# Kernel tuning notes

Measured on AMD Instinct MI355X. Metric: run time of the kernel, lower is better.

## Reference

```python
import jax, jax.numpy as jnp
import numpy as np
import math

FACTOR = 5

def setup_inputs() -> dict:
    key = jax.random.key(0)
    k1, k2, k3, k4 = jax.random.split(key, 4)
    B, L, H, D = 2, 4096, 8, 64
    sample_k = min(FACTOR * int(np.ceil(np.log(L))), L)  # 45
    return {
        "queries": jax.random.normal(k1, (B, L, H, D), dtype=jnp.float32),
        "keys": jax.random.normal(k2, (B, L, H, D), dtype=jnp.float32),
        "values": jax.random.normal(k3, (B, L, H, D), dtype=jnp.float32),
        "attn_mask": jnp.zeros((1,), dtype=bool),  # unused (mask_flag=False)
        "index_sample": jax.random.randint(k4, (L, sample_k), 0, L, dtype=jnp.int64),
    }

def reference(queries, keys, values, attn_mask, index_sample):
    B, L_Q, H, D = queries.shape
    L_K = keys.shape[1]
    # [B,L,H,D] -> [B,H,L,D]
    q = jnp.transpose(queries, (0, 2, 1, 3))
    k = jnp.transpose(keys, (0, 2, 1, 3))
    v = jnp.transpose(values, (0, 2, 1, 3))

    n_top = min(FACTOR * int(np.ceil(np.log(L_Q))), L_Q)  # u

    # --- _prob_QK ---
    # K_sample[b,h,l,s,e] = k[b,h,index_sample[l,s],e]
    K_sample = k[:, :, index_sample, :]                      # [B,H,L_Q,S,E]
    Q_K_sample = jnp.einsum('bhle,bhlse->bhls', q, K_sample)  # [B,H,L_Q,S]
    # sparsity measure: max - mean(over full L_K as in torch code)
    M = Q_K_sample.max(axis=-1) - Q_K_sample.sum(axis=-1) / L_K  # [B,H,L_Q]
    M_top = jax.lax.top_k(M, n_top)[1]                        # [B,H,u] indices

    Q_reduce = jnp.take_along_axis(q, M_top[..., None], axis=2)  # [B,H,u,E]
    scores_top = jnp.einsum('bhue,bhke->bhuk', Q_reduce, k)      # [B,H,u,L_K]

    scale = 1.0 / math.sqrt(D)
    attn = jax.nn.softmax(scale * scores_top, axis=-1)           # [B,H,u,L_K]
    context_in_q = jnp.einsum('bhuk,bhkd->bhud', attn, v)        # [B,H,u,D]

    # scatter selected contexts into zero-initialized tensor
    b_idx = jnp.arange(B)[:, None, None]
    h_idx = jnp.arange(H)[None, :, None]
    context = jnp.zeros((B, H, L_Q, D), dtype=queries.dtype)
    context = context.at[b_idx, h_idx, M_top].set(context_in_q)

    return jnp.transpose(context, (0, 2, 1, 3))  # [B,L_Q,H,D]
```

## Files before the change

### kernel.cpp

```cpp
#include <hip/hip_runtime.h>
#include <math.h>

#define B_ 2
#define L_ 4096
#define H_ 8
#define D_ 64
#define S_ 45
#define NTOP_ 45
#define SCALE 0.125f
#define TKEYS 64
#define NSPLIT 64

template<int CTRL>
__device__ __forceinline__ float dpp_permf(float x) {
    return __int_as_float(__builtin_amdgcn_update_dpp(
        0, __float_as_int(x), CTRL, 0xF, 0xF, true));
}

__global__ __launch_bounds__(256) void compute_M_kernel(
    const float* __restrict__ q, const float* __restrict__ k,
    const int* __restrict__ samp, float* __restrict__ M) {
    __shared__ int sIdx[8 * 48];
    int tid = threadIdx.x;
    int g   = blockIdx.x;
    int xcd = g & 7;
    int chunk = g >> 3;
    int b  = xcd >> 2;
    int h0 = (xcd & 3) * 2;
    int l0 = chunk * 8;

    for (int i = tid; i < 8 * S_; i += 256) {
        int qq = i / S_, ss = i - qq * S_;
        sIdx[qq * 48 + ss] = samp[(long)(l0 + qq) * S_ + ss];
    }
    if (tid < 24) sIdx[(tid / 3) * 48 + S_ + (tid % 3)] = 0;
    __syncthreads();

    int lane = tid & 63, wave = tid >> 6;
    int c  = lane & 31;
    int q8 = wave * 2 + (lane >> 5);
    int l  = l0 + q8;

    float4 q4 = ((const float4*)(q + (((long)(b * L_ + l)) * H_ + h0) * D_))[c];
    const float4* kb4 = (const float4*)(k + ((long)b * L_ * H_ + h0) * (long)D_);
    const int* myIdx = sIdx + q8 * 48;

    float4 f0 = kb4[(long)myIdx[0] * 128 + c];
    float4 f1 = kb4[(long)myIdx[1] * 128 + c];
    float4 f2 = kb4[(long)myIdx[2] * 128 + c];

    float vmax = -INFINITY, vsum = 0.f;
    #pragma unroll 3
    for (int s = 0; s < S_; ++s) {
        float4 nf = kb4[(long)myIdx[s + 3] * 128 + c];
        float p = q4.x * f0.x + q4.y * f0.y + q4.z * f0.z + q4.w * f0.w;
        p += dpp_permf<0xB1>(p);
        p += dpp_permf<0x4E>(p);
        p += __shfl_xor(p, 4, 64);
        p += __shfl_xor(p, 8, 64);
        vmax = fmaxf(vmax, p);
        vsum += p;
        f0 = f1; f1 = f2; f2 = nf;
    }
    if ((lane & 15) == 0) {
        int h = h0 + ((lane >> 4) & 1);
        M[(long)(b * 8 + h) * L_ + l] = vmax - vsum * (1.0f / (float)L_);
    }
}

__global__ __launch_bounds__(256) void chunk_topk_kernel(
    const float* __restrict__ M, unsigned long long* __restrict__ cand) {
    __shared__ unsigned long long sKey[256];
    int g = blockIdx.x;
    int bh = g >> 4, chunk = g & 15;
    int tid = threadIdx.x;
    int l = chunk * 256 + tid;
    unsigned int bts = __float_as_uint(M[(long)bh * L_ + l]);
    unsigned int mapped = bts ^ ((unsigned int)((int)bts >> 31) | 0x80000000u);
    unsigned long long key =
        ((unsigned long long)mapped << 32) | (unsigned long long)(0xFFFFFFFFu - (unsigned int)l);
    sKey[tid] = key;
    __syncthreads();
    int rank = 0;
    #pragma unroll 16
    for (int j = 0; j < 256; ++j)
        rank += (sKey[j] > key) ? 1 : 0;
    if (rank < NTOP_)
        cand[((long)bh * 16 + chunk) * NTOP_ + rank] = key;
}

__global__ __launch_bounds__(256) void merge_topk_kernel(
    const unsigned long long* __restrict__ cand, int* __restrict__ topIdx) {
    __shared__ unsigned long long sKey[16 * NTOP_];
    int bh = blockIdx.x, tid = threadIdx.x;
    for (int i = tid; i < 16 * NTOP_; i += 256)
        sKey[i] = cand[(long)bh * 16 * NTOP_ + i];
    __syncthreads();
    unsigned long long k0 = sKey[tid];
    unsigned long long k1 = sKey[tid + 256];
    bool has2 = (tid + 512) < 16 * NTOP_;
    unsigned long long k2 = has2 ? sKey[tid + 512] : 0ull;
    int r0 = 0, r1 = 0, r2 = 0;
    #pragma unroll 8
    for (int j = 0; j < 16 * NTOP_; ++j) {
        unsigned long long kj = sKey[j];
        r0 += (kj > k0) ? 1 : 0;
        r1 += (kj > k1) ? 1 : 0;
        r2 += (kj > k2) ? 1 : 0;
    }
    int* outRow = topIdx + bh * NTOP_;
    if (r0 < NTOP_) outRow[r0] = (int)(0xFFFFFFFFu - (unsigned int)(k0 & 0xFFFFFFFFull));
    if (r1 < NTOP_) outRow[r1] = (int)(0xFFFFFFFFu - (unsigned int)(k1 & 0xFFFFFFFFull));
    if (has2 && r2 < NTOP_) outRow[r2] = (int)(0xFFFFFFFFu - (unsigned int)(k2 & 0xFFFFFFFFull));
}

#define STRIDE 68
__global__ __launch_bounds__(256, 2) void attn_strip_kernel(
    const float* __restrict__ q, const float* __restrict__ k,
    const float* __restrict__ v, const int* __restrict__ topIdx,
    float* __restrict__ pOut, float* __restrict__ plPart, int nsplit) {
    __shared__ float sQ[48 * STRIDE];
    __shared__ float sK[TKEYS * STRIDE];
    __shared__ float sV[TKEYS * STRIDE];
    __shared__ float sP[48 * STRIDE];

    int g = blockIdx.x;
    int xcd = g & 7;
    int s0 = g >> 3;
    int grp = s0 / nsplit;
    int bh = xcd + 8 * grp;
    int split = s0 - grp * nsplit;
    int b = bh >> 3, h = bh & 7;
    int tid = threadIdx.x;
    int key0 = split * TKEYS;

    #pragma unroll
    for (int j = 0; j < 3; ++j) {
        int i = tid + 256 * j;
        int u = i >> 4, d4 = i & 15;
        float4 val = make_float4(0.f, 0.f, 0.f, 0.f);
        if (u < NTOP_) {
            int lq = topIdx[bh * NTOP_ + u];
            val = *(const float4*)(q + (((long)(b * L_ + lq)) * H_ + h) * D_ + 4 * d4);
        }
        *(float4*)(sQ + u * STRIDE + 4 * d4) = val;
    }
    #pragma unroll
    for (int j = 0; j < 4; ++j) {
        int i = tid + 256 * j;
        int r = i >> 4, d4 = i & 15;
        long off = (((long)(b * L_ + key0 + r)) * H_ + h) * D_ + 4 * d4;
        *(float4*)(sK + r * STRIDE + 4 * d4) = *(const float4*)(k + off);
        *(float4*)(sV + r * STRIDE + 4 * d4) = *(const float4*)(v + off);
    }
    __syncthreads();

    int tx = tid & 15, ty = tid >> 4;
    float acc[3][4];
    #pragma unroll
    for (int i = 0; i < 3; ++i)
        #pragma unroll
        for (int j = 0; j < 4; ++j) acc[i][j] = 0.f;

    #pragma unroll 4
    for (int d4 = 0; d4 < 16; ++d4) {
        float4 qv[3];
        #pragma unroll
        for (int i = 0; i < 3; ++i)
            qv[i] = *(const float4*)(sQ + (3 * ty + i) * STRIDE + 4 * d4);
        #pragma unroll
        for (int j = 0; j < 4; ++j) {
            float4 kv = *(const float4*)(sK + (tx + 16 * j) * STRIDE + 4 * d4);
            #pragma unroll
            for (int i = 0; i < 3; ++i)
                acc[i][j] += qv[i].x * kv.x + qv[i].y * kv.y + qv[i].z * kv.z + qv[i].w * kv.w;
        }
    }
    #pragma unroll
    for (int i = 0; i < 3; ++i) {
        #pragma unroll
        for (int j = 0; j < 4; ++j)
            sP[(3 * ty + i) * STRIDE + tx + 16 * j] = __expf(acc[i][j] * SCALE);
    }
    __syncthreads();

    int dx = tid & 15, uy = tid >> 4;
    float o[3][4];
    float ls[3];
    #pragma unroll
    for (int i = 0; i < 3; ++i) {
        ls[i] = 0.f;
        #pragma unroll
        for (int c = 0; c < 4; ++c) o[i][c] = 0.f;
    }
    #pragma unroll 4
    for (int k4 = 0; k4 < 16; ++k4) {
        float pa[3][4];
        #pragma unroll
        for (int i = 0; i < 3; ++i)
            *(float4*)pa[i] = *(const float4*)(sP + (3 * uy + i) * STRIDE + 4 * k4);
        #pragma unroll
        for (int c = 0; c < 4; ++c) {
            float4 vr = *(const float4*)(sV + (4 * k4 + c) * STRIDE + 4 * dx);
            #pragma unroll
            for (int i = 0; i < 3; ++i) {
                o[i][0] += pa[i][c] * vr.x;
                o[i][1] += pa[i][c] * vr.y;
                o[i][2] += pa[i][c] * vr.z;
                o[i][3] += pa[i][c] * vr.w;
                ls[i]   += pa[i][c];
            }
        }
    }
    #pragma unroll
    for (int i = 0; i < 3; ++i) {
        int u = 3 * uy + i;
        if (u < NTOP_) {
            long base = ((long)(split * 16 + bh) * NTOP_ + u) * D_;
            *(float4*)(pOut + base + 4 * dx) = make_float4(o[i][0], o[i][1], o[i][2], o[i][3]);
            if (dx == 0) plPart[(long)(split * 16 + bh) * NTOP_ + u] = ls[i];
        }
    }
}

__global__ __launch_bounds__(256) void zero_reduce_scatter_kernel(
    const int* __restrict__ topIdx, const float* __restrict__ pOut,
    const float* __restrict__ plPart, float* __restrict__ out, int nsplit) {
    __shared__ int sTop[8 * NTOP_];
    __shared__ int sel[256];
    __shared__ int selCnt;
    int g = blockIdx.x;
    int b = g >> 7;
    int l0 = (g & 127) * 32;
    int tid = threadIdx.x;
    if (tid == 0) selCnt = 0;
    for (int i = tid; i < 8 * NTOP_; i += 256) sTop[i] = topIdx[b * 8 * NTOP_ + i];
    __syncthreads();

    float4* obase = (float4*)(out + ((long)(b * L_ + l0)) * H_ * D_);
    float4 z = make_float4(0.f, 0.f, 0.f, 0.f);
    #pragma unroll
    for (int j = 0; j < 16; ++j) obase[tid + 256 * j] = z;

    {
        int l = l0 + (tid >> 3), h = tid & 7;
        const int* rowp = sTop + h * NTOP_;
        int u = -1;
        #pragma unroll
        for (int t = 0; t < NTOP_; ++t)
            if (rowp[t] == l) u = t;
        if (u >= 0) { int p = atomicAdd(&selCnt, 1); sel[p] = (tid << 8) | u; }
    }
    __syncthreads();

    int lane = tid & 63, wave = tid >> 6;
    int n = selCnt;
    for (int w = wave; w < n; w += 4) {
        int e = sel[w];
        int t = e >> 8, u = e & 255;
        int l = l0 + (t >> 3), h = t & 7, bh = b * 8 + h;
        float lv = (lane < nsplit) ? plPart[((long)lane * 16 + bh) * NTOP_ + u] : 0.f;
        #pragma unroll
        for (int o = 32; o > 0; o >>= 1) lv += __shfl_xor(lv, o, 64);
        float accv = 0.f;
        const float* pb = pOut + ((long)bh * NTOP_ + u) * D_ + lane;
        #pragma unroll 8
        for (int s = 0; s < nsplit; ++s) accv += pb[(long)s * 16 * NTOP_ * D_];
        out[(((long)(b * L_ + l)) * H_ + h) * D_ + lane] = accv / lv;
    }
}

extern "C" void kernel_launch(void* const* d_in, const int* in_sizes, int n_in,
                              void* d_out, int out_size, void* d_ws, size_t ws_size,
                              hipStream_t stream) {
    const float* q = (const float*)d_in[0];
    const float* k = (const float*)d_in[1];
    const float* v = (const float*)d_in[2];
    const int* samp = (const int*)d_in[4];
    float* out = (float*)d_out;

    char* ws = (char*)d_ws;
    const size_t mBytes    = (size_t)B_ * H_ * L_ * sizeof(float);
    const size_t topBytes  = (size_t)B_ * H_ * NTOP_ * sizeof(int);
    const size_t plBytes   = (size_t)NSPLIT * 16 * NTOP_ * sizeof(float);
    const size_t poutBytes = (size_t)NSPLIT * 16 * NTOP_ * D_ * sizeof(float);
    float* M      = (float*)ws;
    int*   topIdx = (int*)(ws + mBytes);
    float* plPart = (float*)(ws + mBytes + topBytes);
    float* pOut   = (float*)(ws + mBytes + topBytes + plBytes);
    unsigned long long* cand =
        (unsigned long long*)(ws + mBytes + topBytes + plBytes + poutBytes);

    int nsplit = NSPLIT;
    while (nsplit > 1) {
        size_t need = mBytes + topBytes + plBytes +
                      (size_t)nsplit * 16 * NTOP_ * D_ * sizeof(float) +
                      (size_t)B_ * H_ * 16 * NTOP_ * sizeof(unsigned long long);
        if (need <= ws_size) break;
        nsplit >>= 1;
    }

    compute_M_kernel<<<4096, 256, 0, stream>>>(q, k, samp, M);

    chunk_topk_kernel<<<B_ * H_ * 16, 256, 0, stream>>>(M, cand);

    merge_topk_kernel<<<B_ * H_, 256, 0, stream>>>(cand, topIdx);

    attn_strip_kernel<<<nsplit * B_ * H_, 256, 0, stream>>>(
        q, k, v, topIdx, pOut, plPart, nsplit);

    zero_reduce_scatter_kernel<<<B_ * (L_ / 32), 256, 0, stream>>>(
        topIdx, pOut, plPart, out, nsplit);
}
```

Measured before the change: 172.6 us.

## Fold top-k merge into attention and reduce kernels, move output zeroing earlier

Removes the standalone merge_topk kernel. Each attention block and each reduce block now redoes the 720-candidate rank merge in shared memory, so the small serial merge launch drops out of the critical path. Zeroing of the output moves into the chunk top-k kernel. The reduce kernel is restructured per (b,h) so it only touches the selected rows and no longer scans for them. The cost is redundant merge work in 1024+64 blocks and extra shared memory in the attention kernel, which may lower occupancy.

```diff
diff --git a/kernel.cpp b/kernel.cpp
--- a/kernel.cpp
+++ b/kernel.cpp
@@ -10,6 +10,7 @@
 #define SCALE 0.125f
 #define TKEYS 64
 #define NSPLIT 64
+#define NCAND (16 * NTOP_)
 
 template<int CTRL>
 __device__ __forceinline__ float dpp_permf(float x) {
@@ -69,11 +70,18 @@
 }
 
 __global__ __launch_bounds__(256) void chunk_topk_kernel(
-    const float* __restrict__ M, unsigned long long* __restrict__ cand) {
+    const float* __restrict__ M, unsigned long long* __restrict__ cand,
+    float* __restrict__ out) {
     __shared__ unsigned long long sKey[256];
     int g = blockIdx.x;
     int bh = g >> 4, chunk = g & 15;
     int tid = threadIdx.x;
+
+    float4 z = make_float4(0.f, 0.f, 0.f, 0.f);
+    float4* obase = (float4*)out + (long)g * 4096 + tid;
+    #pragma unroll
+    for (int j = 0; j < 16; ++j) obase[j * 256] = z;
+
     int l = chunk * 256 + tid;
     unsigned int bts = __float_as_uint(M[(long)bh * L_ + l]);
     unsigned int mapped = bts ^ ((unsigned int)((int)bts >> 31) | 0x80000000u);
@@ -89,40 +97,41 @@
         cand[((long)bh * 16 + chunk) * NTOP_ + rank] = key;
 }
 
-__global__ __launch_bounds__(256) void merge_topk_kernel(
-    const unsigned long long* __restrict__ cand, int* __restrict__ topIdx) {
-    __shared__ unsigned long long sKey[16 * NTOP_];
-    int bh = blockIdx.x, tid = threadIdx.x;
-    for (int i = tid; i < 16 * NTOP_; i += 256)
-        sKey[i] = cand[(long)bh * 16 * NTOP_ + i];
+__device__ __forceinline__ void merge_topk_inline(
+    const unsigned long long* __restrict__ cand, int bh, int tid,
+    unsigned long long* sKey, int* sTop) {
+    for (int i = tid; i < NCAND; i += 256)
+        sKey[i] = cand[(long)bh * NCAND + i];
     __syncthreads();
     unsigned long long k0 = sKey[tid];
     unsigned long long k1 = sKey[tid + 256];
-    bool has2 = (tid + 512) < 16 * NTOP_;
+    bool has2 = (tid + 512) < NCAND;
     unsigned long long k2 = has2 ? sKey[tid + 512] : 0ull;
     int r0 = 0, r1 = 0, r2 = 0;
     #pragma unroll 8
-    for (int j = 0; j < 16 * NTOP_; ++j) {
+    for (int j = 0; j < NCAND; ++j) {
         unsigned long long kj = sKey[j];
         r0 += (kj > k0) ? 1 : 0;
         r1 += (kj > k1) ? 1 : 0;
         r2 += (kj > k2) ? 1 : 0;
     }
-    int* outRow = topIdx + bh * NTOP_;
-    if (r0 < NTOP_) outRow[r0] = (int)(0xFFFFFFFFu - (unsigned int)(k0 & 0xFFFFFFFFull));
-    if (r1 < NTOP_) outRow[r1] = (int)(0xFFFFFFFFu - (unsigned int)(k1 & 0xFFFFFFFFull));
-    if (has2 && r2 < NTOP_) outRow[r2] = (int)(0xFFFFFFFFu - (unsigned int)(k2 & 0xFFFFFFFFull));
+    if (r0 < NTOP_) sTop[r0] = (int)(0xFFFFFFFFu - (unsigned int)(k0 & 0xFFFFFFFFull));
+    if (r1 < NTOP_) sTop[r1] = (int)(0xFFFFFFFFu - (unsigned int)(k1 & 0xFFFFFFFFull));
+    if (has2 && r2 < NTOP_) sTop[r2] = (int)(0xFFFFFFFFu - (unsigned int)(k2 & 0xFFFFFFFFull));
+    __syncthreads();
 }
 
 #define STRIDE 68
 __global__ __launch_bounds__(256, 2) void attn_strip_kernel(
     const float* __restrict__ q, const float* __restrict__ k,
-    const float* __restrict__ v, const int* __restrict__ topIdx,
+    const float* __restrict__ v, const unsigned long long* __restrict__ cand,
     float* __restrict__ pOut, float* __restrict__ plPart, int nsplit) {
     __shared__ float sQ[48 * STRIDE];
     __shared__ float sK[TKEYS * STRIDE];
     __shared__ float sV[TKEYS * STRIDE];
     __shared__ float sP[48 * STRIDE];
+    __shared__ unsigned long long sKey[NCAND];
+    __shared__ int sTop[48];
 
     int g = blockIdx.x;
     int xcd = g & 7;
@@ -135,23 +144,26 @@
     int key0 = split * TKEYS;
 
     #pragma unroll
-    for (int j = 0; j < 3; ++j) {
-        int i = tid + 256 * j;
-        int u = i >> 4, d4 = i & 15;
-        float4 val = make_float4(0.f, 0.f, 0.f, 0.f);
-        if (u < NTOP_) {
-            int lq = topIdx[bh * NTOP_ + u];
-            val = *(const float4*)(q + (((long)(b * L_ + lq)) * H_ + h) * D_ + 4 * d4);
-        }
-        *(float4*)(sQ + u * STRIDE + 4 * d4) = val;
-    }
-    #pragma unroll
     for (int j = 0; j < 4; ++j) {
         int i = tid + 256 * j;
         int r = i >> 4, d4 = i & 15;
         long off = (((long)(b * L_ + key0 + r)) * H_ + h) * D_ + 4 * d4;
         *(float4*)(sK + r * STRIDE + 4 * d4) = *(const float4*)(k + off);
         *(float4*)(sV + r * STRIDE + 4 * d4) = *(const float4*)(v + off);
+    }
+
+    merge_topk_inline(cand, bh, tid, sKey, sTop);
+
+    #pragma unroll
+    for (int j = 0; j < 3; ++j) {
+        int i = tid + 256 * j;
+        int u = i >> 4, d4 = i & 15;
+        float4 val = make_float4(0.f, 0.f, 0.f, 0.f);
+        if (u < NTOP_) {
+            int lq = sTop[u];
+            val = *(const float4*)(q + (((long)(b * L_ + lq)) * H_ + h) * D_ + 4 * d4);
+        }
+        *(float4*)(sQ + u * STRIDE + 4 * d4) = val;
     }
     __syncthreads();
 
@@ -223,42 +235,23 @@
     }
 }
 
-__global__ __launch_bounds__(256) void zero_reduce_scatter_kernel(
-    const int* __restrict__ topIdx, const float* __restrict__ pOut,
+__global__ __launch_bounds__(256) void reduce_scatter_kernel(
+    const unsigned long long* __restrict__ cand, const float* __restrict__ pOut,
     const float* __restrict__ plPart, float* __restrict__ out, int nsplit) {
-    __shared__ int sTop[8 * NTOP_];
-    __shared__ int sel[256];
-    __shared__ int selCnt;
+    __shared__ unsigned long long sKey[NCAND];
+    __shared__ int sTop[48];
     int g = blockIdx.x;
-    int b = g >> 7;
-    int l0 = (g & 127) * 32;
+    int bh = g >> 2, rg = g & 3;
+    int b = bh >> 3, h = bh & 7;
     int tid = threadIdx.x;
-    if (tid == 0) selCnt = 0;
-    for (int i = tid; i < 8 * NTOP_; i += 256) sTop[i] = topIdx[b * 8 * NTOP_ + i];
-    __syncthreads();
-
-    float4* obase = (float4*)(out + ((long)(b * L_ + l0)) * H_ * D_);
-    float4 z = make_float4(0.f, 0.f, 0.f, 0.f);
-    #pragma unroll
-    for (int j = 0; j < 16; ++j) obase[tid + 256 * j] = z;
-
-    {
-        int l = l0 + (tid >> 3), h = tid & 7;
-        const int* rowp = sTop + h * NTOP_;
-        int u = -1;
-        #pragma unroll
-        for (int t = 0; t < NTOP_; ++t)
-            if (rowp[t] == l) u = t;
-        if (u >= 0) { int p = atomicAdd(&selCnt, 1); sel[p] = (tid << 8) | u; }
-    }
-    __syncthreads();
+
+    merge_topk_inline(cand, bh, tid, sKey, sTop);
 
     int lane = tid & 63, wave = tid >> 6;
-    int n = selCnt;
-    for (int w = wave; w < n; w += 4) {
-        int e = sel[w];
-        int t = e >> 8, u = e & 255;
-        int l = l0 + (t >> 3), h = t & 7, bh = b * 8 + h;
+    #pragma unroll
+    for (int it = 0; it < 3; ++it) {
+        int u = rg * 12 + it * 4 + wave;
+        if (u >= NTOP_ || u >= rg * 12 + 12) continue;
         float lv = (lane < nsplit) ? plPart[((long)lane * 16 + bh) * NTOP_ + u] : 0.f;
         #pragma unroll
         for (int o = 32; o > 0; o >>= 1) lv += __shfl_xor(lv, o, 64);
@@ -266,6 +259,7 @@
         const float* pb = pOut + ((long)bh * NTOP_ + u) * D_ + lane;
         #pragma unroll 8
         for (int s = 0; s < nsplit; ++s) accv += pb[(long)s * 16 * NTOP_ * D_];
+        int l = sTop[u];
         out[(((long)(b * L_ + l)) * H_ + h) * D_ + lane] = accv / lv;
     }
 }
@@ -281,34 +275,30 @@
 
     char* ws = (char*)d_ws;
     const size_t mBytes    = (size_t)B_ * H_ * L_ * sizeof(float);
-    const size_t topBytes  = (size_t)B_ * H_ * NTOP_ * sizeof(int);
     const size_t plBytes   = (size_t)NSPLIT * 16 * NTOP_ * sizeof(float);
     const size_t poutBytes = (size_t)NSPLIT * 16 * NTOP_ * D_ * sizeof(float);
+    const size_t candBytes = (size_t)B_ * H_ * NCAND * sizeof(unsigned long long);
     float* M      = (float*)ws;
-    int*   topIdx = (int*)(ws + mBytes);
-    float* plPart = (float*)(ws + mBytes + topBytes);
-    float* pOut   = (float*)(ws + mBytes + topBytes + plBytes);
+    float* plPart = (float*)(ws + mBytes);
+    float* pOut   = (float*)(ws + mBytes + plBytes);
     unsigned long long* cand =
-        (unsigned long long*)(ws + mBytes + topBytes + plBytes + poutBytes);
+        (unsigned long long*)(ws + mBytes + plBytes + poutBytes);
 
     int nsplit = NSPLIT;
     while (nsplit > 1) {
-        size_t need = mBytes + topBytes + plBytes +
-                      (size_t)nsplit * 16 * NTOP_ * D_ * sizeof(float) +
-                      (size_t)B_ * H_ * 16 * NTOP_ * sizeof(unsigned long long);
+        size_t need = mBytes + plBytes + candBytes +
+                      (size_t)nsplit * 16 * NTOP_ * D_ * sizeof(float);
         if (need <= ws_size) break;
         nsplit >>= 1;
     }
 
     compute_M_kernel<<<4096, 256, 0, stream>>>(q, k, samp, M);
 
-    chunk_topk_kernel<<<B_ * H_ * 16, 256, 0, stream>>>(M, cand);
-
-    merge_topk_kernel<<<B_ * H_, 256, 0, stream>>>(cand, topIdx);
+    chunk_topk_kernel<<<B_ * H_ * 16, 256, 0, stream>>>(M, cand, out);
 
     attn_strip_kernel<<<nsplit * B_ * H_, 256, 0, stream>>>(
-        q, k, v, topIdx, pOut, plPart, nsplit);
-
-    zero_reduce_scatter_kernel<<<B_ * (L_ / 32), 256, 0, stream>>>(
-        topIdx, pOut, plPart, out, nsplit);
-}
+        q, k, v, cand, pOut, plPart, nsplit);
+
+    reduce_scatter_kernel<<<B_ * H_ * 4, 256, 0, stream>>>(
+        cand, pOut, plPart, out, nsplit);
+}
```

New measurement: 217.3 us. 25.9% more time.
